# Kernel tuning notes

Measured on AMD Instinct MI355X. Metric: run time of the kernel, lower is better.

The kernel has to match this reference:

```python
import jax, jax.numpy as jnp
import numpy as np

N_NODES = 100000
N_EDGES = 1600000


def gcn_norm(row, col, num_nodes):
    # deg = bincount(row); norm_e = deg^{-1/2}[row] * deg^{-1/2}[col]
    deg = jax.ops.segment_sum(jnp.ones_like(row, dtype=jnp.float32), row,
                              num_segments=num_nodes)
    deg_inv_sqrt = 1.0 / jnp.sqrt(deg + 1e-12)
    return deg_inv_sqrt[row] * deg_inv_sqrt[col]


def graph_conv(x, row, col, norm, W):
    # H = A_norm @ (X W): gather by col, scale by edge norm, scatter-add by row
    xW = x @ W                                   # [N, out]
    msg = xW[col] * norm[:, None]                # [E, out]
    return jax.ops.segment_sum(msg, row, num_segments=x.shape[0])


def setup_inputs() -> dict:
    key = jax.random.key(0)
    k1, k2, k3, k4, k5 = jax.random.split(key, 5)
    x = jax.random.normal(k1, (N_NODES, 32), dtype=jnp.float32)
    edge_index = jax.random.randint(k2, (2, N_EDGES), 0, N_NODES, dtype=jnp.int64)
    W1 = jax.random.normal(k3, (32, 48), dtype=jnp.float32) * (1.0 / np.sqrt(32))
    W2 = jax.random.normal(k4, (48, 48), dtype=jnp.float32) * (1.0 / np.sqrt(48))
    W_out = jax.random.normal(k5, (48, 8), dtype=jnp.float32) * (1.0 / np.sqrt(48))
    return {"x": x, "edge_index": edge_index, "W1": W1, "W2": W2, "W_out": W_out}


def reference(x, edge_index, W1, W2, W_out):
    row, col = edge_index[0], edge_index[1]
    norm = gcn_norm(row, col, x.shape[0])
    h = jax.nn.relu(graph_conv(x, row, col, norm, W1))
    h = jax.nn.relu(graph_conv(h, row, col, norm, W2))
    return graph_conv(h, row, col, norm, W_out)
```

## Files before the change

### kernel.cpp

```cpp
#include <hip/hip_runtime.h>
#include <hip/hip_bf16.h>
#include <cstdint>
#include <cstddef>

static constexpr int NN = 100000;
static constexpr int NE = 1600000;
static constexpr int NB = 391;
static constexpr int GB = 250;
static constexpr int CHUNK = NE / GB;

typedef __attribute__((ext_vector_type(8))) short bf16x8;
typedef __attribute__((ext_vector_type(4))) float f32x4;

static __device__ __forceinline__ unsigned short f2bf(float f) {
  unsigned u = __float_as_uint(f);
  unsigned r = (u + 0x7fffu + ((u >> 16) & 1u)) >> 16;
  return (unsigned short)r;
}


__global__ __launch_bounds__(256) void k_hist(const int* __restrict__ row,
                                              int* __restrict__ counts) {
  __shared__ int hist[NB];
  for (int k = threadIdx.x; k < NB; k += 256) hist[k] = 0;
  __syncthreads();
  int g = blockIdx.x;
  int start = g * CHUNK;
  for (int gi = threadIdx.x; gi < CHUNK / 4; gi += 256) {
    int4 r4 = *reinterpret_cast<const int4*>(row + start + gi * 4);
    atomicAdd(&hist[r4.x >> 8], 1);
    atomicAdd(&hist[r4.y >> 8], 1);
    atomicAdd(&hist[r4.z >> 8], 1);
    atomicAdd(&hist[r4.w >> 8], 1);
  }
  __syncthreads();
  for (int k = threadIdx.x; k < NB; k += 256) counts[k * GB + g] = hist[k];
}


__global__ __launch_bounds__(256) void k_scanA(int* __restrict__ counts,
                                               int* __restrict__ totals) {
  __shared__ int s[256];
  int k = blockIdx.x;
  int i = threadIdx.x;
  int v = (i < GB) ? counts[k * GB + i] : 0;
  s[i] = v;
  __syncthreads();
  for (int off = 1; off < 256; off <<= 1) {
    int t = (i >= off) ? s[i - off] : 0;
    __syncthreads();
    s[i] += t;
    __syncthreads();
  }
  if (i < GB) counts[k * GB + i] = s[i] - v;
  if (i == 255) totals[k] = s[255];
}


__global__ __launch_bounds__(256) void k_scanB(const int* __restrict__ totals,
                                               int* __restrict__ bases, int nb) {
  __shared__ int s[256];
  __shared__ int carry;
  if (threadIdx.x == 0) carry = 0;
  __syncthreads();
  for (int base = 0; base < nb; base += 256) {
    int i = base + threadIdx.x;
    int v = (i < nb) ? totals[i] : 0;
    s[threadIdx.x] = v;
    __syncthreads();
    for (int off = 1; off < 256; off <<= 1) {
      int t = (threadIdx.x >= off) ? s[threadIdx.x - off] : 0;
      __syncthreads();
      s[threadIdx.x] += t;
      __syncthreads();
    }
    int exc = carry + s[threadIdx.x] - v;
    if (i < nb) bases[i] = exc;
    int tile_total = s[255];
    __syncthreads();
    if (threadIdx.x == 0) carry += tile_total;
    __syncthreads();
  }
  if (threadIdx.x == 0) bases[nb] = carry;
}


__global__ __launch_bounds__(256) void k_bucket(const int* __restrict__ row,
                                                const int* __restrict__ col,
                                                const int* __restrict__ counts,
                                                const int* __restrict__ bases,
                                                unsigned int* __restrict__ packed) {
  __shared__ int cur[NB];
  int g = blockIdx.x;
  for (int k = threadIdx.x; k < NB; k += 256)
    cur[k] = bases[k] + counts[k * GB + g];
  __syncthreads();
  int start = g * CHUNK;
  for (int gi = threadIdx.x; gi < CHUNK / 4; gi += 256) {
    int4 r4 = *reinterpret_cast<const int4*>(row + start + gi * 4);
    int4 c4 = *reinterpret_cast<const int4*>(col + start + gi * 4);
    int p0 = atomicAdd(&cur[r4.x >> 8], 1);
    int p1 = atomicAdd(&cur[r4.y >> 8], 1);
    int p2 = atomicAdd(&cur[r4.z >> 8], 1);
    int p3 = atomicAdd(&cur[r4.w >> 8], 1);
    packed[p0] = ((unsigned)(r4.x & 255) << 17) | (unsigned)c4.x;
    packed[p1] = ((unsigned)(r4.y & 255) << 17) | (unsigned)c4.y;
    packed[p2] = ((unsigned)(r4.z & 255) << 17) | (unsigned)c4.z;
    packed[p3] = ((unsigned)(r4.w & 255) << 17) | (unsigned)c4.w;
  }
}


__global__ __launch_bounds__(256) void k_csr(const unsigned int* __restrict__ packed,
                                             const int* __restrict__ bases,
                                             int* __restrict__ rowptr,
                                             float* __restrict__ dis,
                                             int* __restrict__ csr_col,
                                             const float* __restrict__ x,
                                             unsigned short* __restrict__ xb,
                                             int N, int E) {
  __shared__ int rh[256];
  __shared__ int sc[256];
  __shared__ int cur[256];
  __shared__ float ldis[256];
  int b = blockIdx.x;
  int start = bases[b];
  int end = bases[b + 1];

  rh[threadIdx.x] = 0;
  __syncthreads();
  for (int i = start + threadIdx.x; i < end; i += 256)
    atomicAdd(&rh[packed[i] >> 17], 1);
  __syncthreads();

  int v = rh[threadIdx.x];
  sc[threadIdx.x] = v;
  __syncthreads();
  for (int off = 1; off < 256; off <<= 1) {
    int t = (threadIdx.x >= off) ? sc[threadIdx.x - off] : 0;
    __syncthreads();
    sc[threadIdx.x] += t;
    __syncthreads();
  }
  int exc = sc[threadIdx.x] - v;

  float dv = 1.0f / sqrtf((float)v + 1e-12f);
  ldis[threadIdx.x] = dv;
  int gr = (b << 8) + threadIdx.x;
  if (gr < N) {
    rowptr[gr] = start + exc;
    dis[gr] = dv;
  }
  if (b == NB - 1 && threadIdx.x == 0) rowptr[N] = E;

  cur[threadIdx.x] = exc;
  __syncthreads();
  for (int i = start + threadIdx.x; i < end; i += 256) {
    unsigned p = packed[i];
    int lr = p >> 17;
    int c = (int)(p & 0x1FFFFu);
    int pos = atomicAdd(&cur[lr], 1);
    csr_col[start + pos] = c;
  }

  int rows = min(256, N - (b << 8));
  if (rows > 0) {
    const float4* xs = reinterpret_cast<const float4*>(x + ((size_t)b << 8) * 32);
    ushort4* xd = reinterpret_cast<ushort4*>(xb + ((size_t)b << 8) * 32);
    for (int i = threadIdx.x; i < rows * 8; i += 256) {
      float ds = ldis[i >> 3];
      float4 vv = xs[i];
      xd[i] = make_ushort4(f2bf(vv.x * ds), f2bf(vv.y * ds),
                           f2bf(vv.z * ds), f2bf(vv.w * ds));
    }
  }
}


template <int SQ>
static __device__ __forceinline__ void acc_bf(float* acc, const uint4* u) {
#pragma unroll
  for (int q = 0; q < SQ; ++q) {
    acc[8 * q + 0] += __uint_as_float(u[q].x << 16);
    acc[8 * q + 1] += __uint_as_float(u[q].x & 0xffff0000u);
    acc[8 * q + 2] += __uint_as_float(u[q].y << 16);
    acc[8 * q + 3] += __uint_as_float(u[q].y & 0xffff0000u);
    acc[8 * q + 4] += __uint_as_float(u[q].z << 16);
    acc[8 * q + 5] += __uint_as_float(u[q].z & 0xffff0000u);
    acc[8 * q + 6] += __uint_as_float(u[q].w << 16);
    acc[8 * q + 7] += __uint_as_float(u[q].w & 0xffff0000u);
  }
}


__global__ __launch_bounds__(256) void k_gather_bf1(const uint4* __restrict__ src,
                                                    const int* __restrict__ rowptr,
                                                    const int* __restrict__ csr_col,
                                                    const float* __restrict__ dis,
                                                    unsigned short* __restrict__ dst,
                                                    int N) {
  int t = blockIdx.x * 256 + threadIdx.x;
  int r = t >> 2, g = t & 3;
  if (r >= N) return;
  int j = rowptr[r], end = rowptr[r + 1];

  float acc[8];
#pragma unroll
  for (int q = 0; q < 8; ++q) acc[q] = 0.f;

  for (; j + 4 <= end; j += 4) {
    int c0 = csr_col[j], c1 = csr_col[j + 1], c2 = csr_col[j + 2], c3 = csr_col[j + 3];
    uint4 u0 = src[(size_t)c0 * 4 + g];
    uint4 u1 = src[(size_t)c1 * 4 + g];
    uint4 u2 = src[(size_t)c2 * 4 + g];
    uint4 u3 = src[(size_t)c3 * 4 + g];
    acc_bf<1>(acc, &u0);
    acc_bf<1>(acc, &u1);
    acc_bf<1>(acc, &u2);
    acc_bf<1>(acc, &u3);
  }
  for (; j < end; ++j) {
    uint4 u0 = src[(size_t)csr_col[j] * 4 + g];
    acc_bf<1>(acc, &u0);
  }

  float ds = dis[r];
  uint4 pk;
  unsigned* pw = reinterpret_cast<unsigned*>(&pk);
#pragma unroll
  for (int i = 0; i < 4; ++i)
    pw[i] = (unsigned)f2bf(ds * acc[2 * i]) |
            ((unsigned)f2bf(ds * acc[2 * i + 1]) << 16);
  *reinterpret_cast<uint4*>(dst + (size_t)r * 32 + g * 8) = pk;
}


__global__ __launch_bounds__(256) void k_gemm12_mfma(
    const unsigned short* __restrict__ g1b,
    const float* __restrict__ W1,
    const float* __restrict__ W2,
    const float* __restrict__ dis,
    unsigned short* __restrict__ s2,
    int N) {
  __shared__ __align__(16) unsigned short hl[4][16][72];

  int w = threadIdx.x >> 6;
  int l = threadIdx.x & 63;
  int c = l & 15;
  int g = l >> 4;
  int rb = blockIdx.x * 64 + w * 16;
  int r = rb + c;
  int rc = min(r, N - 1);

  bf16x8 w1f[3];
#pragma unroll
  for (int t = 0; t < 3; ++t) {
#pragma unroll
    for (int i = 0; i < 8; ++i)
      w1f[t][i] = (short)f2bf(W1[(g * 8 + i) * 48 + 16 * t + c]);
  }
  bf16x8 w2f[3][2];
#pragma unroll
  for (int t = 0; t < 3; ++t) {
#pragma unroll
    for (int s = 0; s < 2; ++s) {
#pragma unroll
      for (int i = 0; i < 8; ++i) {
        int k = s * 32 + g * 8 + i;
        w2f[t][s][i] = (k < 48) ? (short)f2bf(W2[k * 48 + 16 * t + c]) : (short)0;
      }
    }
  }

  bf16x8 bfr = *reinterpret_cast<const bf16x8*>(g1b + (size_t)rc * 32 + g * 8);
  f32x4 a1[3];
#pragma unroll
  for (int t = 0; t < 3; ++t) {
    a1[t] = f32x4{0.f, 0.f, 0.f, 0.f};
    a1[t] = __builtin_amdgcn_mfma_f32_16x16x32_bf16(w1f[t], bfr, a1[t], 0, 0, 0);
  }

#pragma unroll
  for (int t = 0; t < 3; ++t) {
    int f = 16 * t + 4 * g;
    unsigned p0 = (unsigned)f2bf(fmaxf(a1[t][0], 0.f)) |
                  ((unsigned)f2bf(fmaxf(a1[t][1], 0.f)) << 16);
    unsigned p1 = (unsigned)f2bf(fmaxf(a1[t][2], 0.f)) |
                  ((unsigned)f2bf(fmaxf(a1[t][3], 0.f)) << 16);
    *reinterpret_cast<unsigned*>(&hl[w][c][f]) = p0;
    *reinterpret_cast<unsigned*>(&hl[w][c][f + 2]) = p1;
  }
  *reinterpret_cast<unsigned*>(&hl[w][c][48 + 4 * g]) = 0u;
  *reinterpret_cast<unsigned*>(&hl[w][c][48 + 4 * g + 2]) = 0u;

  f32x4 a2[3];
#pragma unroll
  for (int t = 0; t < 3; ++t) a2[t] = f32x4{0.f, 0.f, 0.f, 0.f};
#pragma unroll
  for (int s = 0; s < 2; ++s) {
    bf16x8 hb = *reinterpret_cast<const bf16x8*>(&hl[w][c][s * 32 + 8 * g]);
#pragma unroll
    for (int t = 0; t < 3; ++t)
      a2[t] = __builtin_amdgcn_mfma_f32_16x16x32_bf16(w2f[t][s], hb, a2[t], 0, 0, 0);
  }

  float ds = dis[rc];
#pragma unroll
  for (int t = 0; t < 3; ++t) {
    int f = 16 * t + 4 * g;
    unsigned p0 = (unsigned)f2bf(ds * a2[t][0]) |
                  ((unsigned)f2bf(ds * a2[t][1]) << 16);
    unsigned p1 = (unsigned)f2bf(ds * a2[t][2]) |
                  ((unsigned)f2bf(ds * a2[t][3]) << 16);
    *reinterpret_cast<unsigned*>(&hl[w][c][f]) = p0;
    *reinterpret_cast<unsigned*>(&hl[w][c][f + 2]) = p1;
  }
#pragma unroll
  for (int h2 = 0; h2 < 2; ++h2) {
    int q = l + 64 * h2;
    int rowq = q >> 3, off = q & 7;
    int rr = rb + rowq;
    if (rr < N) {
      uint4 v = *reinterpret_cast<const uint4*>(&hl[w][rowq][off * 8]);
      *reinterpret_cast<uint4*>(s2 + (size_t)rr * 64 + off * 8) = v;
    }
  }
}


__global__ __launch_bounds__(256) void k_gather_fc(const uint4* __restrict__ src,
                                                   const int* __restrict__ rowptr,
                                                   const int* __restrict__ csr_col,
                                                   const float* __restrict__ dis,
                                                   const float* __restrict__ Wo,
                                                   float* __restrict__ s3, int N) {
  __shared__ float Wol[8 * 68];
  for (int i = threadIdx.x; i < 8 * 68; i += 256) {
    int gg = i / 68, off = i - gg * 68;
    float v = 0.f;
    if (off < 64) {
      int rowf = gg * 8 + (off >> 3);
      if (rowf < 48) v = Wo[rowf * 8 + (off & 7)];
    }
    Wol[i] = v;
  }
  __syncthreads();

  int t = blockIdx.x * 256 + threadIdx.x;
  int r = t >> 3, g = t & 7;
  if (r >= N) return;
  int j = rowptr[r], end = rowptr[r + 1];

  float acc[8];
#pragma unroll
  for (int q = 0; q < 8; ++q) acc[q] = 0.f;

  for (; j + 4 <= end; j += 4) {
    int c0 = csr_col[j], c1 = csr_col[j + 1], c2 = csr_col[j + 2], c3 = csr_col[j + 3];
    uint4 u0 = src[(size_t)c0 * 8 + g];
    uint4 u1 = src[(size_t)c1 * 8 + g];
    uint4 u2 = src[(size_t)c2 * 8 + g];
    uint4 u3 = src[(size_t)c3 * 8 + g];
    acc_bf<1>(acc, &u0);
    acc_bf<1>(acc, &u1);
    acc_bf<1>(acc, &u2);
    acc_bf<1>(acc, &u3);
  }
  for (; j < end; ++j) {
    uint4 u0 = src[(size_t)csr_col[j] * 8 + g];
    acc_bf<1>(acc, &u0);
  }

  float ds = dis[r];
  float v[8];
#pragma unroll
  for (int q = 0; q < 8; ++q) v[q] = fmaxf(ds * acc[q], 0.f);

  float p[8];
#pragma unroll
  for (int n = 0; n < 8; ++n) p[n] = 0.f;
  const float* wbase = &Wol[g * 68];
#pragma unroll
  for (int q = 0; q < 8; ++q) {
    float4 w0 = *reinterpret_cast<const float4*>(wbase + q * 8);
    float4 w1 = *reinterpret_cast<const float4*>(wbase + q * 8 + 4);
    p[0] = fmaf(v[q], w0.x, p[0]);
    p[1] = fmaf(v[q], w0.y, p[1]);
    p[2] = fmaf(v[q], w0.z, p[2]);
    p[3] = fmaf(v[q], w0.w, p[3]);
    p[4] = fmaf(v[q], w1.x, p[4]);
    p[5] = fmaf(v[q], w1.y, p[5]);
    p[6] = fmaf(v[q], w1.z, p[6]);
    p[7] = fmaf(v[q], w1.w, p[7]);
  }
#pragma unroll
  for (int m = 1; m < 8; m <<= 1) {
#pragma unroll
    for (int n = 0; n < 8; ++n) p[n] += __shfl_xor(p[n], m, 64);
  }
  if (g < 2) {
    float4 w = make_float4(ds * p[4 * g + 0], ds * p[4 * g + 1],
                           ds * p[4 * g + 2], ds * p[4 * g + 3]);
    *reinterpret_cast<float4*>(s3 + (size_t)r * 8 + 4 * g) = w;
  }
}


template <int LPR, int FQ>
__global__ __launch_bounds__(256) void k_gather(const float* __restrict__ src,
                                                const int* __restrict__ rowptr,
                                                const int* __restrict__ csr_col,
                                                const float* __restrict__ dis,
                                                float* __restrict__ dst, int N) {
  constexpr int F = LPR * FQ * 4;
  int t = blockIdx.x * 256 + threadIdx.x;
  int r = t / LPR, g = t % LPR;
  if (r >= N) return;
  int j = rowptr[r], end = rowptr[r + 1];

  float acc[FQ * 4];
#pragma unroll
  for (int q = 0; q < FQ * 4; ++q) acc[q] = 0.f;

  for (; j + 2 <= end; j += 2) {
    int c0 = csr_col[j], c1 = csr_col[j + 1];
    const float4* sp0 =
        reinterpret_cast<const float4*>(src + (size_t)c0 * F + g * (FQ * 4));
    const float4* sp1 =
        reinterpret_cast<const float4*>(src + (size_t)c1 * F + g * (FQ * 4));
    float4 v0[FQ], v1[FQ];
#pragma unroll
    for (int q = 0; q < FQ; ++q) v0[q] = sp0[q];
#pragma unroll
    for (int q = 0; q < FQ; ++q) v1[q] = sp1[q];
#pragma unroll
    for (int q = 0; q < FQ; ++q) {
      acc[4 * q + 0] += v0[q].x + v1[q].x;
      acc[4 * q + 1] += v0[q].y + v1[q].y;
      acc[4 * q + 2] += v0[q].z + v1[q].z;
      acc[4 * q + 3] += v0[q].w + v1[q].w;
    }
  }
  if (j < end) {
    int c0 = csr_col[j];
    const float4* sp0 =
        reinterpret_cast<const float4*>(src + (size_t)c0 * F + g * (FQ * 4));
#pragma unroll
    for (int q = 0; q < FQ; ++q) {
      float4 v = sp0[q];
      acc[4 * q + 0] += v.x;
      acc[4 * q + 1] += v.y;
      acc[4 * q + 2] += v.z;
      acc[4 * q + 3] += v.w;
    }
  }

  float ds = dis[r];
  float4* dp = reinterpret_cast<float4*>(dst + (size_t)r * F + g * (FQ * 4));
#pragma unroll
  for (int q = 0; q < FQ; ++q)
    dp[q] = make_float4(ds * acc[4 * q + 0], ds * acc[4 * q + 1],
                        ds * acc[4 * q + 2], ds * acc[4 * q + 3]);
}


extern "C" void kernel_launch(void* const* d_in, const int* in_sizes, int n_in,
                              void* d_out, int out_size, void* d_ws, size_t ws_size,
                              hipStream_t stream) {
  const float* x  = (const float*)d_in[0];
  const int*   ei = (const int*)d_in[1];
  const float* W1 = (const float*)d_in[2];
  const float* W2 = (const float*)d_in[3];
  const float* Wo = (const float*)d_in[4];
  float* out = (float*)d_out;

  const int N = NN, E = NE;
  const int* row = ei;
  const int* col = ei + E;

  int*   counts  = (int*)d_ws;
  int*   totals  = counts + 97760;
  int*   bases   = totals + 416;
  int*   rowptr  = bases + 416;
  float* dis     = (float*)(rowptr + 100032);
  int*   csr_col = (int*)(dis + 100000);
  float* A1      = (float*)(csr_col + NE);
  float* A2      = A1 + 3200000;
  float* s3      = A2 + 4000000;
  unsigned int*   packed = (unsigned int*)A1;
  unsigned short* s2     = (unsigned short*)A1;
  unsigned short* g1b    = (unsigned short*)A2;
  unsigned short* xb     = (unsigned short*)(A2 + 3200000);

  k_hist<<<GB, 256, 0, stream>>>(row, counts);
  k_scanA<<<NB, 256, 0, stream>>>(counts, totals);
  k_scanB<<<1, 256, 0, stream>>>(totals, bases, NB);
  k_bucket<<<GB, 256, 0, stream>>>(row, col, counts, bases, packed);
  k_csr<<<NB, 256, 0, stream>>>(packed, bases, rowptr, dis, csr_col, x, xb, N, E);

  k_gather_bf1<<<(N * 4 + 255) / 256, 256, 0, stream>>>(
      (const uint4*)xb, rowptr, csr_col, dis, g1b, N);

  k_gemm12_mfma<<<(N + 63) / 64, 256, 0, stream>>>(g1b, W1, W2, dis, s2, N);

  k_gather_fc<<<(N * 8 + 255) / 256, 256, 0, stream>>>(
      (const uint4*)s2, rowptr, csr_col, dis, Wo, s3, N);

  k_gather<2, 1><<<(N * 2 + 255) / 256, 256, 0, stream>>>(s3, rowptr, csr_col,
                                                          dis, out, N);
}
```

Baseline: 131.7 us.

## Fuse first gather into GEMM, inline bases scan, store final-layer features as bf16

The single-block scanB kernel is removed: each bucket and CSR block now scans the 391 per-bucket totals redundantly in shared memory. The first-layer gather is fused into the MFMA GEMM kernel through a shared-memory tile, so the g1 intermediate never goes to global memory. The last-layer features s3 are stored as bf16 and gathered with one thread per row using 16-byte loads. Together these cut two kernel launches and some global traffic, at the cost of redundant scan work per block, lower precision in the final layer, and possibly lower occupancy in the fused kernel.

```diff
diff --git a/kernel.cpp b/kernel.cpp
--- a/kernel.cpp
+++ b/kernel.cpp
@@ -57,43 +57,47 @@
 }
 
 
-__global__ __launch_bounds__(256) void k_scanB(const int* __restrict__ totals,
-                                               int* __restrict__ bases, int nb) {
-  __shared__ int s[256];
-  __shared__ int carry;
-  if (threadIdx.x == 0) carry = 0;
-  __syncthreads();
-  for (int base = 0; base < nb; base += 256) {
+static __device__ __forceinline__ void scan_totals(const int* __restrict__ totals,
+                                                   int* bases_l, int* ss,
+                                                   int* carry_p) {
+  if (threadIdx.x == 0) *carry_p = 0;
+  __syncthreads();
+  for (int base = 0; base < NB; base += 256) {
     int i = base + threadIdx.x;
-    int v = (i < nb) ? totals[i] : 0;
-    s[threadIdx.x] = v;
+    int v = (i < NB) ? totals[i] : 0;
+    ss[threadIdx.x] = v;
     __syncthreads();
     for (int off = 1; off < 256; off <<= 1) {
-      int t = (threadIdx.x >= off) ? s[threadIdx.x - off] : 0;
+      int t = (threadIdx.x >= off) ? ss[threadIdx.x - off] : 0;
       __syncthreads();
-      s[threadIdx.x] += t;
+      ss[threadIdx.x] += t;
       __syncthreads();
     }
-    int exc = carry + s[threadIdx.x] - v;
-    if (i < nb) bases[i] = exc;
-    int tile_total = s[255];
-    __syncthreads();
-    if (threadIdx.x == 0) carry += tile_total;
-    __syncthreads();
-  }
-  if (threadIdx.x == 0) bases[nb] = carry;
+    if (i < NB) bases_l[i] = *carry_p + ss[threadIdx.x] - v;
+    int tile_total = ss[255];
+    __syncthreads();
+    if (threadIdx.x == 0) *carry_p += tile_total;
+    __syncthreads();
+  }
+  if (threadIdx.x == 0) bases_l[NB] = *carry_p;
+  __syncthreads();
 }
 
 
 __global__ __launch_bounds__(256) void k_bucket(const int* __restrict__ row,
                                                 const int* __restrict__ col,
                                                 const int* __restrict__ counts,
-                                                const int* __restrict__ bases,
+                                                const int* __restrict__ totals,
                                                 unsigned int* __restrict__ packed) {
   __shared__ int cur[NB];
+  __shared__ int bases_l[NB + 1];
+  __shared__ int ss[256];
+  __shared__ int carry;
+  scan_totals(totals, bases_l, ss, &carry);
+
   int g = blockIdx.x;
   for (int k = threadIdx.x; k < NB; k += 256)
-    cur[k] = bases[k] + counts[k * GB + g];
+    cur[k] = bases_l[k] + counts[k * GB + g];
   __syncthreads();
   int start = g * CHUNK;
   for (int gi = threadIdx.x; gi < CHUNK / 4; gi += 256) {
@@ -112,20 +116,24 @@
 
 
 __global__ __launch_bounds__(256) void k_csr(const unsigned int* __restrict__ packed,
-                                             const int* __restrict__ bases,
+                                             const int* __restrict__ totals,
                                              int* __restrict__ rowptr,
                                              float* __restrict__ dis,
                                              int* __restrict__ csr_col,
                                              const float* __restrict__ x,
                                              unsigned short* __restrict__ xb,
                                              int N, int E) {
+  __shared__ int bases_l[NB + 1];
+  __shared__ int ss[256];
+  __shared__ int carry;
   __shared__ int rh[256];
-  __shared__ int sc[256];
   __shared__ int cur[256];
   __shared__ float ldis[256];
+  scan_totals(totals, bases_l, ss, &carry);
+
   int b = blockIdx.x;
-  int start = bases[b];
-  int end = bases[b + 1];
+  int start = bases_l[b];
+  int end = bases_l[b + 1];
 
   rh[threadIdx.x] = 0;
   __syncthreads();
@@ -134,15 +142,15 @@
   __syncthreads();
 
   int v = rh[threadIdx.x];
-  sc[threadIdx.x] = v;
+  ss[threadIdx.x] = v;
   __syncthreads();
   for (int off = 1; off < 256; off <<= 1) {
-    int t = (threadIdx.x >= off) ? sc[threadIdx.x - off] : 0;
-    __syncthreads();
-    sc[threadIdx.x] += t;
-    __syncthreads();
-  }
-  int exc = sc[threadIdx.x] - v;
+    int t = (threadIdx.x >= off) ? ss[threadIdx.x - off] : 0;
+    __syncthreads();
+    ss[threadIdx.x] += t;
+    __syncthreads();
+  }
+  int exc = ss[threadIdx.x] - v;
 
   float dv = 1.0f / sqrtf((float)v + 1e-12f);
   ldis[threadIdx.x] = dv;
@@ -193,62 +201,61 @@
 }
 
 
-__global__ __launch_bounds__(256) void k_gather_bf1(const uint4* __restrict__ src,
-                                                    const int* __restrict__ rowptr,
-                                                    const int* __restrict__ csr_col,
-                                                    const float* __restrict__ dis,
-                                                    unsigned short* __restrict__ dst,
-                                                    int N) {
-  int t = blockIdx.x * 256 + threadIdx.x;
-  int r = t >> 2, g = t & 3;
-  if (r >= N) return;
-  int j = rowptr[r], end = rowptr[r + 1];
-
-  float acc[8];
-#pragma unroll
-  for (int q = 0; q < 8; ++q) acc[q] = 0.f;
-
-  for (; j + 4 <= end; j += 4) {
-    int c0 = csr_col[j], c1 = csr_col[j + 1], c2 = csr_col[j + 2], c3 = csr_col[j + 3];
-    uint4 u0 = src[(size_t)c0 * 4 + g];
-    uint4 u1 = src[(size_t)c1 * 4 + g];
-    uint4 u2 = src[(size_t)c2 * 4 + g];
-    uint4 u3 = src[(size_t)c3 * 4 + g];
-    acc_bf<1>(acc, &u0);
-    acc_bf<1>(acc, &u1);
-    acc_bf<1>(acc, &u2);
-    acc_bf<1>(acc, &u3);
-  }
-  for (; j < end; ++j) {
-    uint4 u0 = src[(size_t)csr_col[j] * 4 + g];
-    acc_bf<1>(acc, &u0);
-  }
-
-  float ds = dis[r];
-  uint4 pk;
-  unsigned* pw = reinterpret_cast<unsigned*>(&pk);
-#pragma unroll
-  for (int i = 0; i < 4; ++i)
-    pw[i] = (unsigned)f2bf(ds * acc[2 * i]) |
-            ((unsigned)f2bf(ds * acc[2 * i + 1]) << 16);
-  *reinterpret_cast<uint4*>(dst + (size_t)r * 32 + g * 8) = pk;
-}
-
-
-__global__ __launch_bounds__(256) void k_gemm12_mfma(
-    const unsigned short* __restrict__ g1b,
+__global__ __launch_bounds__(256) void k_g1gemm(
+    const uint4* __restrict__ src,
+    const int* __restrict__ rowptr,
+    const int* __restrict__ csr_col,
+    const float* __restrict__ dis,
     const float* __restrict__ W1,
     const float* __restrict__ W2,
-    const float* __restrict__ dis,
     unsigned short* __restrict__ s2,
     int N) {
+  __shared__ __align__(16) unsigned short g1l[64][36];
   __shared__ __align__(16) unsigned short hl[4][16][72];
+
+  int rb0 = blockIdx.x * 64;
+
+  {
+    int lr = threadIdx.x >> 2, gg = threadIdx.x & 3;
+    int r = rb0 + lr;
+    uint4 pk = make_uint4(0u, 0u, 0u, 0u);
+    if (r < N) {
+      int j = rowptr[r], end = rowptr[r + 1];
+      float acc[8];
+#pragma unroll
+      for (int q = 0; q < 8; ++q) acc[q] = 0.f;
+      for (; j + 4 <= end; j += 4) {
+        int c0 = csr_col[j], c1 = csr_col[j + 1];
+        int c2 = csr_col[j + 2], c3 = csr_col[j + 3];
+        uint4 u0 = src[(size_t)c0 * 4 + gg];
+        uint4 u1 = src[(size_t)c1 * 4 + gg];
+        uint4 u2 = src[(size_t)c2 * 4 + gg];
+        uint4 u3 = src[(size_t)c3 * 4 + gg];
+        acc_bf<1>(acc, &u0);
+        acc_bf<1>(acc, &u1);
+        acc_bf<1>(acc, &u2);
+        acc_bf<1>(acc, &u3);
+      }
+      for (; j < end; ++j) {
+        uint4 u0 = src[(size_t)csr_col[j] * 4 + gg];
+        acc_bf<1>(acc, &u0);
+      }
+      float ds = dis[r];
+      unsigned* pw = reinterpret_cast<unsigned*>(&pk);
+#pragma unroll
+      for (int i = 0; i < 4; ++i)
+        pw[i] = (unsigned)f2bf(ds * acc[2 * i]) |
+                ((unsigned)f2bf(ds * acc[2 * i + 1]) << 16);
+    }
+    *reinterpret_cast<uint4*>(&g1l[lr][gg * 8]) = pk;
+  }
+  __syncthreads();
 
   int w = threadIdx.x >> 6;
   int l = threadIdx.x & 63;
   int c = l & 15;
   int g = l >> 4;
-  int rb = blockIdx.x * 64 + w * 16;
+  int rb = rb0 + w * 16;
   int r = rb + c;
   int rc = min(r, N - 1);
 
@@ -272,7 +279,7 @@
     }
   }
 
-  bf16x8 bfr = *reinterpret_cast<const bf16x8*>(g1b + (size_t)rc * 32 + g * 8);
+  bf16x8 bfr = *reinterpret_cast<const bf16x8*>(&g1l[w * 16 + c][g * 8]);
   f32x4 a1[3];
 #pragma unroll
   for (int t = 0; t < 3; ++t) {
@@ -333,7 +340,8 @@
                                                    const int* __restrict__ csr_col,
                                                    const float* __restrict__ dis,
                                                    const float* __restrict__ Wo,
-                                                   float* __restrict__ s3, int N) {
+                                                   unsigned short* __restrict__ s3b,
+                                                   int N) {
   __shared__ float Wol[8 * 68];
   for (int i = threadIdx.x; i < 8 * 68; i += 256) {
     int gg = i / 68, off = i - gg * 68;
@@ -398,69 +406,51 @@
 #pragma unroll
     for (int n = 0; n < 8; ++n) p[n] += __shfl_xor(p[n], m, 64);
   }
-  if (g < 2) {
-    float4 w = make_float4(ds * p[4 * g + 0], ds * p[4 * g + 1],
-                           ds * p[4 * g + 2], ds * p[4 * g + 3]);
-    *reinterpret_cast<float4*>(s3 + (size_t)r * 8 + 4 * g) = w;
-  }
-}
-
-
-template <int LPR, int FQ>
-__global__ __launch_bounds__(256) void k_gather(const float* __restrict__ src,
-                                                const int* __restrict__ rowptr,
-                                                const int* __restrict__ csr_col,
-                                                const float* __restrict__ dis,
-                                                float* __restrict__ dst, int N) {
-  constexpr int F = LPR * FQ * 4;
-  int t = blockIdx.x * 256 + threadIdx.x;
-  int r = t / LPR, g = t % LPR;
+  if (g == 0) {
+    uint4 pk;
+    unsigned* pw = reinterpret_cast<unsigned*>(&pk);
+#pragma unroll
+    for (int i = 0; i < 4; ++i)
+      pw[i] = (unsigned)f2bf(ds * p[2 * i]) |
+              ((unsigned)f2bf(ds * p[2 * i + 1]) << 16);
+    *reinterpret_cast<uint4*>(s3b + (size_t)r * 8) = pk;
+  }
+}
+
+
+__global__ __launch_bounds__(256) void k_gather_s3(const uint4* __restrict__ src,
+                                                   const int* __restrict__ rowptr,
+                                                   const int* __restrict__ csr_col,
+                                                   const float* __restrict__ dis,
+                                                   float* __restrict__ out, int N) {
+  int r = blockIdx.x * 256 + threadIdx.x;
   if (r >= N) return;
   int j = rowptr[r], end = rowptr[r + 1];
 
-  float acc[FQ * 4];
-#pragma unroll
-  for (int q = 0; q < FQ * 4; ++q) acc[q] = 0.f;
-
-  for (; j + 2 <= end; j += 2) {
-    int c0 = csr_col[j], c1 = csr_col[j + 1];
-    const float4* sp0 =
-        reinterpret_cast<const float4*>(src + (size_t)c0 * F + g * (FQ * 4));
-    const float4* sp1 =
-        reinterpret_cast<const float4*>(src + (size_t)c1 * F + g * (FQ * 4));
-    float4 v0[FQ], v1[FQ];
-#pragma unroll
-    for (int q = 0; q < FQ; ++q) v0[q] = sp0[q];
-#pragma unroll
-    for (int q = 0; q < FQ; ++q) v1[q] = sp1[q];
-#pragma unroll
-    for (int q = 0; q < FQ; ++q) {
-      acc[4 * q + 0] += v0[q].x + v1[q].x;
-      acc[4 * q + 1] += v0[q].y + v1[q].y;
-      acc[4 * q + 2] += v0[q].z + v1[q].z;
-      acc[4 * q + 3] += v0[q].w + v1[q].w;
-    }
-  }
-  if (j < end) {
-    int c0 = csr_col[j];
-    const float4* sp0 =
-        reinterpret_cast<const float4*>(src + (size_t)c0 * F + g * (FQ * 4));
-#pragma unroll
-    for (int q = 0; q < FQ; ++q) {
-      float4 v = sp0[q];
-      acc[4 * q + 0] += v.x;
-      acc[4 * q + 1] += v.y;
-      acc[4 * q + 2] += v.z;
-      acc[4 * q + 3] += v.w;
-    }
+  float acc[8];
+#pragma unroll
+  for (int q = 0; q < 8; ++q) acc[q] = 0.f;
+
+  for (; j + 4 <= end; j += 4) {
+    int c0 = csr_col[j], c1 = csr_col[j + 1], c2 = csr_col[j + 2], c3 = csr_col[j + 3];
+    uint4 u0 = src[c0];
+    uint4 u1 = src[c1];
+    uint4 u2 = src[c2];
+    uint4 u3 = src[c3];
+    acc_bf<1>(acc, &u0);
+    acc_bf<1>(acc, &u1);
+    acc_bf<1>(acc, &u2);
+    acc_bf<1>(acc, &u3);
+  }
+  for (; j < end; ++j) {
+    uint4 u0 = src[csr_col[j]];
+    acc_bf<1>(acc, &u0);
   }
 
   float ds = dis[r];
-  float4* dp = reinterpret_cast<float4*>(dst + (size_t)r * F + g * (FQ * 4));
-#pragma unroll
-  for (int q = 0; q < FQ; ++q)
-    dp[q] = make_float4(ds * acc[4 * q + 0], ds * acc[4 * q + 1],
-                        ds * acc[4 * q + 2], ds * acc[4 * q + 3]);
+  float4* dp = reinterpret_cast<float4*>(out + (size_t)r * 8);
+  dp[0] = make_float4(ds * acc[0], ds * acc[1], ds * acc[2], ds * acc[3]);
+  dp[1] = make_float4(ds * acc[4], ds * acc[5], ds * acc[6], ds * acc[7]);
 }
 
 
@@ -480,32 +470,26 @@
 
   int*   counts  = (int*)d_ws;
   int*   totals  = counts + 97760;
-  int*   bases   = totals + 416;
-  int*   rowptr  = bases + 416;
+  int*   rowptr  = totals + 416;
   float* dis     = (float*)(rowptr + 100032);
   int*   csr_col = (int*)(dis + 100000);
   float* A1      = (float*)(csr_col + NE);
-  float* A2      = A1 + 3200000;
-  float* s3      = A2 + 4000000;
+  unsigned short* xb  = (unsigned short*)(A1 + 3200000);
+  unsigned short* s3b = (unsigned short*)(A1 + 4800000);
   unsigned int*   packed = (unsigned int*)A1;
   unsigned short* s2     = (unsigned short*)A1;
-  unsigned short* g1b    = (unsigned short*)A2;
-  unsigned short* xb     = (unsigned short*)(A2 + 3200000);
 
   k_hist<<<GB, 256, 0, stream>>>(row, counts);
   k_scanA<<<NB, 256, 0, stream>>>(counts, totals);
-  k_scanB<<<1, 256, 0, stream>>>(totals, bases, NB);
-  k_bucket<<<GB, 256, 0, stream>>>(row, col, counts, bases, packed);
-  k_csr<<<NB, 256, 0, stream>>>(packed, bases, rowptr, dis, csr_col, x, xb, N, E);
-
-  k_gather_bf1<<<(N * 4 + 255) / 256, 256, 0, stream>>>(
-      (const uint4*)xb, rowptr, csr_col, dis, g1b, N);
-
-  k_gemm12_mfma<<<(N + 63) / 64, 256, 0, stream>>>(g1b, W1, W2, dis, s2, N);
+  k_bucket<<<GB, 256, 0, stream>>>(row, col, counts, totals, packed);
+  k_csr<<<NB, 256, 0, stream>>>(packed, totals, rowptr, dis, csr_col, x, xb, N, E);
+
+  k_g1gemm<<<(N + 63) / 64, 256, 0, stream>>>(
+      (const uint4*)xb, rowptr, csr_col, dis, W1, W2, s2, N);
 
   k_gather_fc<<<(N * 8 + 255) / 256, 256, 0, stream>>>(
-      (const uint4*)s2, rowptr, csr_col, dis, Wo, s3, N);
-
-  k_gather<2, 1><<<(N * 2 + 255) / 256, 256, 0, stream>>>(s3, rowptr, csr_col,
-                                                          dis, out, N);
-}
+      (const uint4*)s2, rowptr, csr_col, dis, Wo, s3b, N);
+
+  k_gather_s3<<<(N + 255) / 256, 256, 0, stream>>>(
+      (const uint4*)s3b, rowptr, csr_col, dis, out, N);
+}
```

Result: faster. 125.2 us (median of 2 runs) (-4.9%).
